# Kernel optimization log

Measured on AMD Instinct MI355X. Metric: run time of the kernel, lower is better.

The kernel has to match this reference:

```python
import jax, jax.numpy as jnp
import numpy as np

EMBED_DIM = 1024
NUM_HEADS = 16
HEAD_DIM = EMBED_DIM // NUM_HEADS
B, S = 4, 2048


def setup_inputs() -> dict:
    key = jax.random.key(0)
    ks = jax.random.split(key, 9)
    scale = 1.0 / np.sqrt(EMBED_DIM)
    inp = {
        "inputs": jax.random.normal(ks[0], (B, S, EMBED_DIM), dtype=jnp.float32),
        "rotation_params": jax.random.normal(ks[1], (B, S, EMBED_DIM), dtype=jnp.float32),
        "entangle_params": jax.random.normal(ks[2], (B, S, EMBED_DIM), dtype=jnp.float32),
        # Linear weights stored as (out, in) like torch; applied as x @ W.T
        "Wq": jax.random.normal(ks[3], (EMBED_DIM, EMBED_DIM), dtype=jnp.float32) * scale,
        "Wk": jax.random.normal(ks[4], (EMBED_DIM, EMBED_DIM), dtype=jnp.float32) * scale,
        "Wv": jax.random.normal(ks[5], (EMBED_DIM, EMBED_DIM), dtype=jnp.float32) * scale,
        "Wrot": jax.random.normal(ks[6], (EMBED_DIM, EMBED_DIM), dtype=jnp.float32) * scale,
        "Went": jax.random.normal(ks[7], (EMBED_DIM, EMBED_DIM), dtype=jnp.float32) * scale,
        "Wo": jax.random.normal(ks[8], (EMBED_DIM, EMBED_DIM), dtype=jnp.float32) * scale,
    }
    return inp


def _split_heads(x):
    b, s, e = x.shape
    return x.reshape(b, s, NUM_HEADS, HEAD_DIM).transpose(0, 2, 1, 3)  # (B,H,S,D)


def reference(inputs, rotation_params, entangle_params, Wq, Wk, Wv, Wrot, Went, Wo):
    Q = inputs @ Wq.T + rotation_params @ Wrot.T
    K = inputs @ Wk.T + entangle_params @ Went.T
    V = inputs @ Wv.T
    Qh, Kh, Vh = _split_heads(Q), _split_heads(K), _split_heads(V)
    scores = jnp.einsum("bhqd,bhkd->bhqk", Qh, Kh) / jnp.sqrt(jnp.float32(HEAD_DIM))
    attn = jax.nn.softmax(scores, axis=-1)  # dropout p=0 -> identity
    out = jnp.einsum("bhqk,bhkd->bhqd", attn, Vh)
    out = out.transpose(0, 2, 1, 3).reshape(inputs.shape[0], inputs.shape[1], EMBED_DIM)
    return out @ Wo.T
```

## Files before the change

kernel.cpp:

```cpp
#include <hip/hip_runtime.h>
#include <stdint.h>


typedef unsigned short u16;
typedef __bf16 bf16x8 __attribute__((ext_vector_type(8)));
typedef float f32x4 __attribute__((ext_vector_type(4)));
typedef float f32x16 __attribute__((ext_vector_type(16)));
typedef uint32_t u32x4 __attribute__((ext_vector_type(4)));

#define MFMA_BF16(a, b, c) __builtin_amdgcn_mfma_f32_16x16x32_bf16((a), (b), (c), 0, 0, 0)
#define MFMA32(a, b, c)    __builtin_amdgcn_mfma_f32_32x32x16_bf16((a), (b), (c), 0, 0, 0)
#define GAMMA 0.18033688011112042f
#define BHSTRIDE 131072
#define FENCE() __builtin_amdgcn_sched_barrier(0)

static __device__ __forceinline__ u16 f2bf(float f) {
    uint32_t u = __builtin_bit_cast(uint32_t, f);
    u = (u + 0x7FFFu + ((u >> 16) & 1u)) >> 16;
    return (u16)u;
}

static __device__ __forceinline__ uint32_t pk_rne2(float a, float b) {
    uint32_t ua = __builtin_bit_cast(uint32_t, a);
    uint32_t ub = __builtin_bit_cast(uint32_t, b);
    ua += 0x7FFFu + ((ua >> 16) & 1u);
    ub += 0x7FFFu + ((ub >> 16) & 1u);
    return __builtin_amdgcn_perm(ub, ua, 0x07060302);
}

static __device__ __forceinline__ void async_copy16(const void* g, void* l) {
    __builtin_amdgcn_global_load_lds((__attribute__((address_space(1))) void*)g,
                                     (__attribute__((address_space(3))) void*)l,
                                     16, 0, 0);
}

static __device__ __forceinline__ float aexp2(float x) {
    float r;
    asm("v_exp_f32 %0, %1" : "=v"(r) : "v"(x));
    return r;
}

static __device__ __forceinline__ uint32_t cvtpk(float a, float b) {
    uint32_t r;
    asm("v_cvt_pk_bf16_f32 %0, %1, %2" : "=v"(r) : "v"(a), "v"(b));
    return r;
}

static __device__ __forceinline__ void plswap(uint32_t& a, uint32_t& b) {
    asm("v_permlane32_swap_b32 %0, %1" : "+v"(a), "+v"(b));
}

static __device__ __forceinline__ bf16x8 mkfrag(uint32_t w0, uint32_t w1,
                                                uint32_t w2, uint32_t w3) {
    u32x4 u = {w0, w1, w2, w3};
    return __builtin_bit_cast(bf16x8, u);
}

struct CvtArgs { const float* s[6]; u16* d[6]; };

__global__ __launch_bounds__(256) void cvt_kernel(CvtArgs a, int nelem) {
    const float* s = a.s[blockIdx.z];
    u16* d = a.d[blockIdx.z];
    int i = (blockIdx.x * 256 + threadIdx.x) * 8;
    float4 f0 = *(const float4*)(s + i);
    float4 f1 = *(const float4*)(s + i + 4);
    uint4 w;
    w.x = pk_rne2(f0.x, f0.y); w.y = pk_rne2(f0.z, f0.w);
    w.z = pk_rne2(f1.x, f1.y); w.w = pk_rne2(f1.z, f1.w);
    *(uint4*)(d + i) = w;
}

template <int AMODE, int CMODE>
__global__ __launch_bounds__(256, 2) void gemm_bt(
    const u16* __restrict__ A0, const u16* __restrict__ W0,
    const u16* __restrict__ A1, const u16* __restrict__ W1,
    void* __restrict__ Cv, int K, int npairs, float scale)
{
    __shared__ __align__(16) u16 lA[128 * 64];
    __shared__ __align__(16) u16 lB[128 * 64];

    const int tid  = threadIdx.x;
    const int lane = tid & 63;
    const int wave = tid >> 6;
    const int wm   = (wave >> 1) * 64;
    const int wn   = (wave & 1) * 64;
    const size_t m0 = (size_t)blockIdx.x * 128;
    const size_t n0 = (size_t)blockIdx.y * 128;

    const int row8 = tid >> 3;
    const int cp   = tid & 7;
    const int fr   = lane & 15;
    const int g    = lane >> 4;

    const size_t bb = (m0 >> 11) * 16;
    const size_t s0 = m0 & 2047;

    f32x4 acc[4][4] = {};

    for (int p = 0; p < npairs; ++p) {
        const u16* A = p ? A1 : A0;
        const u16* W = p ? W1 : W0;
        for (int k0 = 0; k0 < K; k0 += 64) {
            __syncthreads();
#pragma unroll
            for (int it = 0; it < 4; ++it) {
                int row = it * 32 + row8;
                int sc = cp ^ (((row >> 3) ^ row) & 7);
                if (AMODE == 0) {
                    async_copy16(A + ((m0 + row) * (size_t)K + k0 + sc * 8),
                                 (char*)lA + it * 4096 + tid * 16);
                } else {
                    size_t base = (bb + (size_t)(k0 >> 6)) * BHSTRIDE;
                    async_copy16(A + base + (s0 + row) * 64 + sc * 8,
                                 (char*)lA + it * 4096 + tid * 16);
                }
                async_copy16(W + ((n0 + row) * (size_t)K + k0 + sc * 8),
                             (char*)lB + it * 4096 + tid * 16);
            }
            __syncthreads();

            bf16x8 af[4][2], bfm[4][2];
#pragma unroll
            for (int i = 0; i < 4; ++i) {
                int row = wm + i * 16 + fr;
                int sw = ((row >> 3) ^ row) & 7;
                af[i][0] = *(const bf16x8*)(lA + row * 64 + (g ^ sw) * 8);
                af[i][1] = *(const bf16x8*)(lA + row * 64 + ((4 + g) ^ sw) * 8);
            }
#pragma unroll
            for (int j = 0; j < 4; ++j) {
                int row = wn + j * 16 + fr;
                int sw = ((row >> 3) ^ row) & 7;
                bfm[j][0] = *(const bf16x8*)(lB + row * 64 + (g ^ sw) * 8);
                bfm[j][1] = *(const bf16x8*)(lB + row * 64 + ((4 + g) ^ sw) * 8);
            }
#pragma unroll
            for (int i = 0; i < 4; ++i)
#pragma unroll
                for (int j = 0; j < 4; ++j) {
                    acc[i][j] = MFMA_BF16(af[i][0], bfm[j][0], acc[i][j]);
                    acc[i][j] = MFMA_BF16(af[i][1], bfm[j][1], acc[i][j]);
                }
        }
    }

#pragma unroll
    for (int i = 0; i < 4; ++i)
#pragma unroll
        for (int j = 0; j < 4; ++j) {
            if (CMODE == 2) {
                size_t row0 = m0 + wm + i * 16 + g * 4;
                size_t col  = n0 + wn + j * 16 + fr;
                size_t addr = ((row0 >> 11) * 16 + (col >> 6)) * BHSTRIDE
                            + (size_t)(col & 63) * 2048 + (row0 & 2047);
                ushort4 pk;
                pk.x = f2bf(acc[i][j][0] * scale);
                pk.y = f2bf(acc[i][j][1] * scale);
                pk.z = f2bf(acc[i][j][2] * scale);
                pk.w = f2bf(acc[i][j][3] * scale);
                *(ushort4*)((u16*)Cv + addr) = pk;
            } else {
#pragma unroll
                for (int rg = 0; rg < 4; ++rg) {
                    size_t row = m0 + wm + i * 16 + g * 4 + rg;
                    size_t col = n0 + wn + j * 16 + fr;
                    float v = acc[i][j][rg] * scale;
                    if (CMODE == 0) {
                        ((float*)Cv)[row * 1024 + col] = v;
                    } else {
                        size_t addr = ((row >> 11) * 16 + (col >> 6)) * BHSTRIDE
                                    + (row & 2047) * 64 + (col & 63);
                        ((u16*)Cv)[addr] = f2bf(v);
                    }
                }
            }
        }
}

__global__ __launch_bounds__(256, 2) void flash_kernel(
    const u16* __restrict__ Qhm, const u16* __restrict__ Khm,
    const u16* __restrict__ Vt, u16* __restrict__ Ohm)
{
    __shared__ __align__(16) u16 sK[2][128 * 64];
    __shared__ __align__(16) u16 sVt[2][64 * 128];

    const int tid  = threadIdx.x;
    const int lane = tid & 63;
    const int wave = tid >> 6;
    const int l31  = lane & 31;
    const int hg   = lane >> 5;

    const int lin  = blockIdx.x;
    const int slot = lin >> 3;
    const int bh   = (lin & 7) + 8 * (slot >> 4);
    const int q0   = (slot & 15) * 128;

    const u16* Qh = Qhm + (size_t)bh * BHSTRIDE;
    const u16* Kh = Khm + (size_t)bh * BHSTRIDE;
    const u16* Vh = Vt  + (size_t)bh * BHSTRIDE;
    u16*       Oh = Ohm + (size_t)bh * BHSTRIDE;

    bf16x8 qbf[4];
#pragma unroll
    for (int dc = 0; dc < 4; ++dc)
        qbf[dc] = *(const bf16x8*)(Qh +
            (size_t)(q0 + wave * 32 + l31) * 64 + dc * 16 + hg * 8);

    f32x16 oacc[2] = {};
    float lsum4[4] = {};

    const int krow8 = tid >> 3, kcp = tid & 7;
    const int vd16  = tid >> 4, vcp = tid & 15;

    auto stage = [&](int buf, int kt) {
#pragma unroll
        for (int it = 0; it < 4; ++it) {
            int row = it * 32 + krow8;
            int sc = kcp ^ (((row >> 3) ^ row) & 7);
            async_copy16(Kh + (size_t)(kt * 128 + row) * 64 + sc * 8,
                         (char*)(&sK[buf][0]) + it * 4096 + tid * 16);
        }
#pragma unroll
        for (int it = 0; it < 4; ++it) {
            int d = it * 16 + vd16;
            int sc = vcp ^ (d & 15);
            async_copy16(Vh + (size_t)d * 2048 + kt * 128 + sc * 8,
                         (char*)(&sVt[buf][0]) + it * 4096 + tid * 16);
        }
    };

    auto qk = [&](const u16* sKc, int kc) -> f32x16 {
        f32x16 sa = {};
        const int krow = kc * 32 + l31;
        const int ksw = ((krow >> 3) ^ krow) & 7;
#pragma unroll
        for (int dc = 0; dc < 4; ++dc) {
            bf16x8 ka = *(const bf16x8*)(sKc + krow * 64 + ((dc * 2 + hg) ^ ksw) * 8);
            sa = MFMA32(ka, qbf[dc], sa);
        }
        return sa;
    };

    auto sm = [&](const f32x16& sa, bf16x8& o0, bf16x8& o1) {
        float p[16];
#pragma unroll
        for (int r = 0; r < 16; ++r) p[r] = aexp2(sa[r]);
#pragma unroll
        for (int r = 0; r < 16; ++r) lsum4[r & 3] += p[r];
        uint32_t w0 = cvtpk(p[0],  p[1]),  w1 = cvtpk(p[2],  p[3]);
        uint32_t w2 = cvtpk(p[4],  p[5]),  w3 = cvtpk(p[6],  p[7]);
        uint32_t w4 = cvtpk(p[8],  p[9]),  w5 = cvtpk(p[10], p[11]);
        uint32_t w6 = cvtpk(p[12], p[13]), w7 = cvtpk(p[14], p[15]);
        plswap(w0, w2); plswap(w1, w3);
        plswap(w4, w6); plswap(w5, w7);
        o0 = mkfrag(w0, w1, w2, w3);
        o1 = mkfrag(w4, w5, w6, w7);
    };

    auto pv = [&](const u16* sVc, int kc, bf16x8 pa0, bf16x8 pa1) {
        bf16x8 vb[2][2];
#pragma unroll
        for (int sub = 0; sub < 2; ++sub)
#pragma unroll
            for (int dt = 0; dt < 2; ++dt) {
                int dr = dt * 32 + l31;
                vb[sub][dt] = *(const bf16x8*)(sVc + dr * 128 +
                    ((kc * 4 + sub * 2 + hg) ^ (dr & 15)) * 8);
            }
        oacc[0] = MFMA32(pa0, vb[0][0], oacc[0]);
        oacc[1] = MFMA32(pa0, vb[0][1], oacc[1]);
        oacc[0] = MFMA32(pa1, vb[1][0], oacc[0]);
        oacc[1] = MFMA32(pa1, vb[1][1], oacc[1]);
    };

    stage(0, 0);
    __syncthreads();

    int cur = 0;
    for (int kt = 0; kt < 16; ++kt) {
        const u16* sKc = &sK[cur][0];
        const u16* sVc = &sVt[cur][0];

        f32x16 saA = qk(sKc, 0);
        f32x16 saB = qk(sKc, 1);
        if (kt < 15) stage(cur ^ 1, kt + 1);
        FENCE();

        bf16x8 a0, a1, b0, b1;
        sm(saA, a0, a1);   FENCE();
        saA = qk(sKc, 2);  FENCE();
        pv(sVc, 0, a0, a1); FENCE();
        sm(saB, b0, b1);   FENCE();
        saB = qk(sKc, 3);  FENCE();
        pv(sVc, 1, b0, b1); FENCE();
        sm(saA, a0, a1);   FENCE();
        pv(sVc, 2, a0, a1); FENCE();
        sm(saB, b0, b1);   FENCE();
        pv(sVc, 3, b0, b1);

        __syncthreads();
        cur ^= 1;
    }

    {
        float l = (lsum4[0] + lsum4[1]) + (lsum4[2] + lsum4[3]);
        l += __shfl_xor(l, 32);
        float inv = 1.0f / l;
#pragma unroll
        for (int r = 0; r < 16; ++r) {
            int row = (r & 3) + 4 * hg + 8 * (r >> 2);
            float invr = __shfl(inv, row);
            size_t grow = (size_t)q0 + wave * 32 + row;
            Oh[grow * 64 + l31]      = f2bf(oacc[0][r] * invr);
            Oh[grow * 64 + 32 + l31] = f2bf(oacc[1][r] * invr);
        }
    }
}

extern "C" void kernel_launch(void* const* d_in, const int* in_sizes, int n_in,
                              void* d_out, int out_size, void* d_ws, size_t ws_size,
                              hipStream_t stream)
{
    const float* X    = (const float*)d_in[0];
    const float* R    = (const float*)d_in[1];
    const float* E    = (const float*)d_in[2];
    const float* Wq   = (const float*)d_in[3];
    const float* Wk   = (const float*)d_in[4];
    const float* Wv   = (const float*)d_in[5];
    const float* Wrot = (const float*)d_in[6];
    const float* Went = (const float*)d_in[7];
    const float* Wo   = (const float*)d_in[8];

    const size_t NT = 8192 * 1024;
    const size_t NW = 1024 * 1024;

    u16* Qhm = (u16*)d_out;
    u16* Khm = Qhm + NT;
    u16* Xb  = (u16*)d_ws;
    u16* RVb = Xb + NT;
    u16* EOb = RVb + NT;
    u16* Wqb = EOb + NT;
    u16* Wkb   = Wqb + NW;
    u16* Wvb   = Wkb + NW;
    u16* Wrotb = Wvb + NW;
    u16* Wentb = Wrotb + NW;
    u16* Wob   = Wentb + NW;

    {
        CvtArgs a{};
        a.s[0] = X; a.s[1] = R; a.s[2] = E;
        a.d[0] = Xb; a.d[1] = RVb; a.d[2] = EOb;
        cvt_kernel<<<dim3(4096, 1, 3), 256, 0, stream>>>(a, (int)NT);
    }
    {
        CvtArgs a{};
        a.s[0] = Wq; a.s[1] = Wk; a.s[2] = Wv; a.s[3] = Wrot; a.s[4] = Went; a.s[5] = Wo;
        a.d[0] = Wqb; a.d[1] = Wkb; a.d[2] = Wvb; a.d[3] = Wrotb; a.d[4] = Wentb; a.d[5] = Wob;
        cvt_kernel<<<dim3(512, 1, 6), 256, 0, stream>>>(a, (int)NW);
    }

    dim3 gproj(64, 8);
    gemm_bt<0, 1><<<gproj, 256, 0, stream>>>(Xb, Wqb, RVb, Wrotb, Qhm, 1024, 2, GAMMA);
    gemm_bt<0, 1><<<gproj, 256, 0, stream>>>(Xb, Wkb, EOb, Wentb, Khm, 1024, 2, 1.0f);
    gemm_bt<0, 2><<<gproj, 256, 0, stream>>>(Xb, Wvb, nullptr, nullptr, RVb, 1024, 1, 1.0f);
    flash_kernel<<<dim3(1024), 256, 0, stream>>>(Qhm, Khm, RVb, EOb);
    gemm_bt<1, 0><<<gproj, 256, 0, stream>>>(EOb, Wob, nullptr, nullptr, d_out, 1024, 1, 1.0f);
}
```

Baseline: 367.2 us.

## Double query rows per wave in flash attention to reuse K/V fragments

Each wave now handles two 32-row query tiles (256 query rows per block), so every K fragment and V fragment read from shared memory feeds two MFMAs instead of one. The grid halves to 512 blocks and the softmax/PV schedule is reinterleaved across both tiles. This cuts LDS reads and global K/V staging per unit of work, but doubles the accumulator and Q register footprint and halves the number of blocks. That may reduce occupancy or leave CUs idle.

```diff
diff --git a/kernel.cpp b/kernel.cpp
--- a/kernel.cpp
+++ b/kernel.cpp
@@ -192,22 +192,25 @@
 
     const int lin  = blockIdx.x;
     const int slot = lin >> 3;
-    const int bh   = (lin & 7) + 8 * (slot >> 4);
-    const int q0   = (slot & 15) * 128;
+    const int bh   = (lin & 7) + 8 * (slot >> 3);
+    const int q0   = (slot & 7) * 256;
 
     const u16* Qh = Qhm + (size_t)bh * BHSTRIDE;
     const u16* Kh = Khm + (size_t)bh * BHSTRIDE;
     const u16* Vh = Vt  + (size_t)bh * BHSTRIDE;
     u16*       Oh = Ohm + (size_t)bh * BHSTRIDE;
 
-    bf16x8 qbf[4];
-#pragma unroll
-    for (int dc = 0; dc < 4; ++dc)
-        qbf[dc] = *(const bf16x8*)(Qh +
-            (size_t)(q0 + wave * 32 + l31) * 64 + dc * 16 + hg * 8);
-
-    f32x16 oacc[2] = {};
-    float lsum4[4] = {};
+    bf16x8 qbf[2][4];
+#pragma unroll
+    for (int qt = 0; qt < 2; ++qt)
+#pragma unroll
+        for (int dc = 0; dc < 4; ++dc)
+            qbf[qt][dc] = *(const bf16x8*)(Qh +
+                (size_t)(q0 + wave * 64 + qt * 32 + l31) * 64 + dc * 16 + hg * 8);
+
+    f32x16 oaccA[2] = {};
+    f32x16 oaccB[2] = {};
+    float lsA[2] = {}, lsB[2] = {};
 
     const int krow8 = tid >> 3, kcp = tid & 7;
     const int vd16  = tid >> 4, vcp = tid & 15;
@@ -229,24 +232,25 @@
         }
     };
 
-    auto qk = [&](const u16* sKc, int kc) -> f32x16 {
-        f32x16 sa = {};
+    auto qk2 = [&](const u16* sKc, int kc, f32x16& sa0, f32x16& sa1) {
+        sa0 = (f32x16){};
+        sa1 = (f32x16){};
         const int krow = kc * 32 + l31;
         const int ksw = ((krow >> 3) ^ krow) & 7;
 #pragma unroll
         for (int dc = 0; dc < 4; ++dc) {
             bf16x8 ka = *(const bf16x8*)(sKc + krow * 64 + ((dc * 2 + hg) ^ ksw) * 8);
-            sa = MFMA32(ka, qbf[dc], sa);
-        }
-        return sa;
+            sa0 = MFMA32(ka, qbf[0][dc], sa0);
+            sa1 = MFMA32(ka, qbf[1][dc], sa1);
+        }
     };
 
-    auto sm = [&](const f32x16& sa, bf16x8& o0, bf16x8& o1) {
+    auto sm = [&](const f32x16& sa, bf16x8& o0, bf16x8& o1, float* ls) {
         float p[16];
 #pragma unroll
         for (int r = 0; r < 16; ++r) p[r] = aexp2(sa[r]);
 #pragma unroll
-        for (int r = 0; r < 16; ++r) lsum4[r & 3] += p[r];
+        for (int r = 0; r < 16; ++r) ls[r & 1] += p[r];
         uint32_t w0 = cvtpk(p[0],  p[1]),  w1 = cvtpk(p[2],  p[3]);
         uint32_t w2 = cvtpk(p[4],  p[5]),  w3 = cvtpk(p[6],  p[7]);
         uint32_t w4 = cvtpk(p[8],  p[9]),  w5 = cvtpk(p[10], p[11]);
@@ -257,7 +261,8 @@
         o1 = mkfrag(w4, w5, w6, w7);
     };
 
-    auto pv = [&](const u16* sVc, int kc, bf16x8 pa0, bf16x8 pa1) {
+    auto pv2 = [&](const u16* sVc, int kc, bf16x8 a0, bf16x8 a1,
+                   bf16x8 b0, bf16x8 b1) {
         bf16x8 vb[2][2];
 #pragma unroll
         for (int sub = 0; sub < 2; ++sub)
@@ -267,10 +272,14 @@
                 vb[sub][dt] = *(const bf16x8*)(sVc + dr * 128 +
                     ((kc * 4 + sub * 2 + hg) ^ (dr & 15)) * 8);
             }
-        oacc[0] = MFMA32(pa0, vb[0][0], oacc[0]);
-        oacc[1] = MFMA32(pa0, vb[0][1], oacc[1]);
-        oacc[0] = MFMA32(pa1, vb[1][0], oacc[0]);
-        oacc[1] = MFMA32(pa1, vb[1][1], oacc[1]);
+        oaccA[0] = MFMA32(a0, vb[0][0], oaccA[0]);
+        oaccA[1] = MFMA32(a0, vb[0][1], oaccA[1]);
+        oaccB[0] = MFMA32(b0, vb[0][0], oaccB[0]);
+        oaccB[1] = MFMA32(b0, vb[0][1], oaccB[1]);
+        oaccA[0] = MFMA32(a1, vb[1][0], oaccA[0]);
+        oaccA[1] = MFMA32(a1, vb[1][1], oaccA[1]);
+        oaccB[0] = MFMA32(b1, vb[1][0], oaccB[0]);
+        oaccB[1] = MFMA32(b1, vb[1][1], oaccB[1]);
     };
 
     stage(0, 0);
@@ -281,38 +290,45 @@
         const u16* sKc = &sK[cur][0];
         const u16* sVc = &sVt[cur][0];
 
-        f32x16 saA = qk(sKc, 0);
-        f32x16 saB = qk(sKc, 1);
+        f32x16 sA, sB, nA, nB;
+        qk2(sKc, 0, sA, sB);
         if (kt < 15) stage(cur ^ 1, kt + 1);
         FENCE();
 
         bf16x8 a0, a1, b0, b1;
-        sm(saA, a0, a1);   FENCE();
-        saA = qk(sKc, 2);  FENCE();
-        pv(sVc, 0, a0, a1); FENCE();
-        sm(saB, b0, b1);   FENCE();
-        saB = qk(sKc, 3);  FENCE();
-        pv(sVc, 1, b0, b1); FENCE();
-        sm(saA, a0, a1);   FENCE();
-        pv(sVc, 2, a0, a1); FENCE();
-        sm(saB, b0, b1);   FENCE();
-        pv(sVc, 3, b0, b1);
+        sm(sA, a0, a1, lsA);   FENCE();
+        qk2(sKc, 1, nA, nB);   FENCE();
+        sm(sB, b0, b1, lsB);   FENCE();
+        pv2(sVc, 0, a0, a1, b0, b1); FENCE();
+        sm(nA, a0, a1, lsA);   FENCE();
+        qk2(sKc, 2, sA, sB);   FENCE();
+        sm(nB, b0, b1, lsB);   FENCE();
+        pv2(sVc, 1, a0, a1, b0, b1); FENCE();
+        sm(sA, a0, a1, lsA);   FENCE();
+        qk2(sKc, 3, nA, nB);   FENCE();
+        sm(sB, b0, b1, lsB);   FENCE();
+        pv2(sVc, 2, a0, a1, b0, b1); FENCE();
+        sm(nA, a0, a1, lsA);   FENCE();
+        sm(nB, b0, b1, lsB);   FENCE();
+        pv2(sVc, 3, a0, a1, b0, b1);
 
         __syncthreads();
         cur ^= 1;
     }
 
-    {
-        float l = (lsum4[0] + lsum4[1]) + (lsum4[2] + lsum4[3]);
+#pragma unroll
+    for (int qt = 0; qt < 2; ++qt) {
+        float l = qt ? (lsB[0] + lsB[1]) : (lsA[0] + lsA[1]);
         l += __shfl_xor(l, 32);
         float inv = 1.0f / l;
+        const f32x16* oa = qt ? oaccB : oaccA;
 #pragma unroll
         for (int r = 0; r < 16; ++r) {
             int row = (r & 3) + 4 * hg + 8 * (r >> 2);
             float invr = __shfl(inv, row);
-            size_t grow = (size_t)q0 + wave * 32 + row;
-            Oh[grow * 64 + l31]      = f2bf(oacc[0][r] * invr);
-            Oh[grow * 64 + 32 + l31] = f2bf(oacc[1][r] * invr);
+            size_t grow = (size_t)q0 + wave * 64 + qt * 32 + row;
+            Oh[grow * 64 + l31]      = f2bf(oa[0][r] * invr);
+            Oh[grow * 64 + 32 + l31] = f2bf(oa[1][r] * invr);
         }
     }
 }
@@ -363,6 +379,6 @@
     gemm_bt<0, 1><<<gproj, 256, 0, stream>>>(Xb, Wqb, RVb, Wrotb, Qhm, 1024, 2, GAMMA);
     gemm_bt<0, 1><<<gproj, 256, 0, stream>>>(Xb, Wkb, EOb, Wentb, Khm, 1024, 2, 1.0f);
     gemm_bt<0, 2><<<gproj, 256, 0, stream>>>(Xb, Wvb, nullptr, nullptr, RVb, 1024, 1, 1.0f);
-    flash_kernel<<<dim3(1024), 256, 0, stream>>>(Qhm, Khm, RVb, EOb);
+    flash_kernel<<<dim3(512), 256, 0, stream>>>(Qhm, Khm, RVb, EOb);
     gemm_bt<1, 0><<<gproj, 256, 0, stream>>>(EOb, Wob, nullptr, nullptr, d_out, 1024, 1, 1.0f);
 }
```

New measurement: 369.8 us. About the same (+0.7%).
